# Optimization experiments

Hardware: AMD Instinct MI355X
Metric: run time of the kernel (lower is better)

## Reference

```python
import jax, jax.numpy as jnp
from jax import lax
import numpy as np

B, C, H, W = 32, 3, 224, 224
NUM_CLASSES = 100
K = 3  # kernel size
OUT1 = 32


def _bn(x, g, b, m, v, eps=1e-5):
    # eval-mode batchnorm over channel dim of NCHW
    inv = g / jnp.sqrt(v + eps)
    return x * inv[None, :, None, None] + (b - m * inv)[None, :, None, None]


def _conv(x, w, pad=1):
    return lax.conv_general_dilated(
        x, w, (1, 1), ((pad, pad), (pad, pad)),
        dimension_numbers=('NCHW', 'OIHW', 'NCHW'))


def _maxpool2(x):
    return lax.reduce_window(x, -jnp.inf, lax.max, (1, 1, 2, 2), (1, 1, 2, 2), 'VALID')


def setup_inputs() -> dict:
    key = jax.random.key(0)
    ks = jax.random.split(key, 32)
    n = lambda k, s, sc=0.05: jax.random.normal(k, s, jnp.float32) * sc
    u = lambda k, s: jax.random.uniform(k, s, jnp.float32, 0.5, 1.5)
    inp = {
        'x': jax.random.normal(ks[0], (B, C, H, W), jnp.float32),
        # weight_gen MLP: Linear(3,128)->ReLU->Linear(128,256)->ReLU->Linear(256, 32*3*3*3)
        'w1': n(ks[1], (128, C)), 'b1': n(ks[2], (128,)),
        'w2': n(ks[3], (256, 128)), 'b2': n(ks[4], (256,)),
        'w3': n(ks[5], (OUT1 * C * K * K, 256)), 'b3': n(ks[6], (OUT1 * C * K * K,)),
        # bias_gen: Linear(3, 32)
        'wb': n(ks[7], (OUT1, C)), 'bb': n(ks[8], (OUT1,)),
        'conv2_w': n(ks[9], (64, 32, 3, 3)), 'conv2_b': n(ks[10], (64,)),
        'conv3_w': n(ks[11], (128, 64, 3, 3)), 'conv3_b': n(ks[12], (128,)),
        'bn1_g': 1.0 + n(ks[13], (32,)), 'bn1_b': n(ks[14], (32,)), 'bn1_m': n(ks[15], (32,)), 'bn1_v': u(ks[16], (32,)),
        'bn2_g': 1.0 + n(ks[17], (64,)), 'bn2_b': n(ks[18], (64,)), 'bn2_m': n(ks[19], (64,)), 'bn2_v': u(ks[20], (64,)),
        'bn3_g': 1.0 + n(ks[21], (128,)), 'bn3_b': n(ks[22], (128,)), 'bn3_m': n(ks[23], (128,)), 'bn3_v': u(ks[24], (128,)),
        'fc_w': n(ks[25], (NUM_CLASSES, 128)), 'fc_b': n(ks[26], (NUM_CLASSES,)),
    }
    return inp


def reference(x, w1, b1, w2, b2, w3, b3, wb, bb, conv2_w, conv2_b, conv3_w, conv3_b,
              bn1_g, bn1_b, bn1_m, bn1_v, bn2_g, bn2_b, bn2_m, bn2_v,
              bn3_g, bn3_b, bn3_m, bn3_v, fc_w, fc_b):
    Bx = x.shape[0]
    # DynamicConv2D: channel indicator is all-ones since C == max_in_channels
    ind = jnp.ones((Bx, C), x.dtype)
    h = jax.nn.relu(ind @ w1.T + b1)
    h = jax.nn.relu(h @ w2.T + b2)
    dyn_w = (h @ w3.T + b3).reshape(Bx, OUT1, C, K, K)  # per-sample [O,I,k,k]
    dyn_b = ind @ wb.T + bb                             # per-sample [O]
    # vmap over batch: one single-image conv per sample with its own weights
    y = jax.vmap(lambda xi, wi, bi: _conv(xi[None], wi)[0] + bi[:, None, None])(x, dyn_w, dyn_b)
    y = jax.nn.relu(_bn(y, bn1_g, bn1_b, bn1_m, bn1_v))
    y = _maxpool2(y)
    y = jax.nn.relu(_bn(_conv(y, conv2_w) + conv2_b[None, :, None, None], bn2_g, bn2_b, bn2_m, bn2_v))
    y = _maxpool2(y)
    y = jax.nn.relu(_bn(_conv(y, conv3_w) + conv3_b[None, :, None, None], bn3_g, bn3_b, bn3_m, bn3_v))
    y = y.mean(axis=(2, 3))  # AdaptiveAvgPool2d((1,1)) + flatten
    # dropout is identity in eval
    return y @ fc_w.T + fc_b
```

## Files before the change

kernel.cpp:

```cpp
#include <hip/hip_runtime.h>
#include <hip/hip_bf16.h>

#define BATCH 32
#define HW1 224

typedef __attribute__((ext_vector_type(8))) short short8;
typedef __attribute__((ext_vector_type(4))) float floatx4;

static __device__ __forceinline__ unsigned short f2bf(float f) {
    unsigned int u = __float_as_uint(f);
    unsigned int r = (u + 0x7fffu + ((u >> 16) & 1u)) >> 16;
    return (unsigned short)r;
}

__global__ __launch_bounds__(256) void gen_dynw_repack(
    const float* __restrict__ w1, const float* __restrict__ b1,
    const float* __restrict__ w2, const float* __restrict__ b2,
    const float* __restrict__ w3, const float* __restrict__ b3,
    const float* __restrict__ conv2_w, const float* __restrict__ conv3_w,
    const float* __restrict__ wb, const float* __restrict__ bb,
    const float* __restrict__ conv2_b, const float* __restrict__ conv3_b,
    const float* __restrict__ bn1_g, const float* __restrict__ bn1_b,
    const float* __restrict__ bn1_m, const float* __restrict__ bn1_v,
    const float* __restrict__ bn2_g, const float* __restrict__ bn2_b,
    const float* __restrict__ bn2_m, const float* __restrict__ bn2_v,
    const float* __restrict__ bn3_g, const float* __restrict__ bn3_b,
    const float* __restrict__ bn3_m, const float* __restrict__ bn3_v,
    float* __restrict__ dwt,
    unsigned short* __restrict__ wrep2, unsigned short* __restrict__ wrep3,
    float* __restrict__ bn1_s, float* __restrict__ bn1_t,
    float* __restrict__ bn2_s, float* __restrict__ bn2_t,
    float* __restrict__ bn3_s, float* __restrict__ bn3_t,
    float* __restrict__ feat)
{
    __shared__ float h1s[128];
    __shared__ float h2s[256];
    const int blk = blockIdx.x;
    const int t = threadIdx.x;
    if (blk < 216) {
        if (t < 128) {
            float s = b1[t] + w1[t*3+0] + w1[t*3+1] + w1[t*3+2];
            h1s[t] = fmaxf(s, 0.f);
        }
        __syncthreads();
        {
            float s = b2[t];
            const float* wr = w2 + (size_t)t*128;
#pragma unroll 4
            for (int k = 0; k < 128; k += 4) {
                float4 wv = *(const float4*)(wr + k);
                s = fmaf(wv.x, h1s[k  ], s);
                s = fmaf(wv.y, h1s[k+1], s);
                s = fmaf(wv.z, h1s[k+2], s);
                s = fmaf(wv.w, h1s[k+3], s);
            }
            h2s[t] = fmaxf(s, 0.f);
        }
        __syncthreads();
        const int wave = t >> 6, lane = t & 63;
        const int row = blk*4 + wave;
        float4 wv = *(const float4*)(w3 + (size_t)row*256 + lane*4);
        float4 hv = *(const float4*)&h2s[lane*4];
        float s = wv.x*hv.x + wv.y*hv.y + wv.z*hv.z + wv.w*hv.w;
#pragma unroll
        for (int m = 1; m < 64; m <<= 1) s += __shfl_xor(s, m);
        if (lane == 0) {
            int oc = row / 27, tap = row - oc*27;
            dwt[tap*32 + oc] = s + b3[row];
        }
    } else if (blk < 576) {
        const int i = (blk - 216)*256 + t;
        const int N2 = 9*64*32;
        if (i < N2) {
            int tp = i / (64*32); int rem = i - tp*(64*32);
            int oc = rem >> 5, ic = rem & 31;
            wrep2[i] = f2bf(conv2_w[(oc*32 + ic)*9 + tp]);
        } else {
            int j = i - N2;
            int tp = j / (128*64); int rem = j - tp*(128*64);
            int oc = rem >> 6, ic = rem & 63;
            wrep3[j] = f2bf(conv3_w[(oc*64 + ic)*9 + tp]);
        }
    } else {
        if (t < 32) {
            float dynb = bb[t] + wb[t*3+0] + wb[t*3+1] + wb[t*3+2];
            float s = bn1_g[t] / sqrtf(bn1_v[t] + 1e-5f);
            bn1_s[t] = s;
            bn1_t[t] = (dynb - bn1_m[t]) * s + bn1_b[t];
        }
        if (t < 64) {
            float s = bn2_g[t] / sqrtf(bn2_v[t] + 1e-5f);
            bn2_s[t] = s;
            bn2_t[t] = (conv2_b[t] - bn2_m[t]) * s + bn2_b[t];
        }
        if (t < 128) {
            float s = bn3_g[t] / sqrtf(bn3_v[t] + 1e-5f);
            bn3_s[t] = s;
            bn3_t[t] = (conv3_b[t] - bn3_m[t]) * s + bn3_b[t];
        }
        for (int i = t; i < BATCH*128; i += 256) feat[i] = 0.f;
    }
}

__global__ __launch_bounds__(256) void conv1_pool(
    const float* __restrict__ x, const float* __restrict__ dwt,
    const float* __restrict__ bn_s, const float* __restrict__ bn_t,
    unsigned short* __restrict__ act1)
{
    __shared__ __align__(16) unsigned short sp[18*18*4];
    __shared__ __align__(16) unsigned short swA[32*32];
    __shared__ __align__(16) unsigned short swB[32*32];

    const int tid = threadIdx.x;
    const int bx = blockIdx.x, by = blockIdx.y, b = blockIdx.z;
    const int gx0 = bx*16 - 1, gy0 = by*16 - 1;
    const float* xb = x + (size_t)b * 3 * HW1 * HW1;

    for (int i = tid; i < 1024; i += 256) { swA[i] = 0; swB[i] = 0; }

    for (int i = tid; i < 324; i += 256) {
        int r = i / 18, c = i - r*18;
        int gy = gy0 + r, gx = gx0 + c;
        unsigned short v0 = 0, v1 = 0, v2 = 0;
        if ((unsigned)gy < HW1 && (unsigned)gx < HW1) {
            const float* pp = xb + gy*HW1 + gx;
            v0 = f2bf(pp[0]);
            v1 = f2bf(pp[HW1*HW1]);
            v2 = f2bf(pp[2*HW1*HW1]);
        }
        unsigned int lo = (unsigned int)v0 | ((unsigned int)v1 << 16);
        unsigned int hi = (unsigned int)v2;
        *(uint2*)&sp[i*4] = make_uint2(lo, hi);
    }
    __syncthreads();

    for (int i = tid; i < 864; i += 256) {
        int tap = i >> 5, oc = i & 31;
        int ic = tap / 9, kk = tap - ic*9;
        int ky = kk / 3, kx = kk - ky*3;
        unsigned short v = f2bf(dwt[i]);
        if (kk == 8)      swB[oc*32 + ic] = v;
        else if (kx < 2)  swA[oc*32 + ky*8 + kx*4 + ic] = v;
        else              swA[oc*32 + 3*8  + ky*4 + ic] = v;
    }
    __syncthreads();

    const int lane = tid & 63, wave = tid >> 6;
    const int n = lane & 15, quad = lane >> 4;

    short8 afrA[2], afrB[2];
#pragma unroll
    for (int h = 0; h < 2; ++h) {
        afrA[h] = *(const short8*)&swA[((h*16 + n)*32) + quad*8];
        afrB[h] = *(const short8*)&swB[((h*16 + n)*32) + quad*8];
    }
    float4 sv[2], tv[2];
#pragma unroll
    for (int h = 0; h < 2; ++h) {
        sv[h] = *(const float4*)(bn_s + h*16 + quad*4);
        tv[h] = *(const float4*)(bn_t + h*16 + quad*4);
    }

    union U { short8 s8; uint2 u2[2]; };

    const int y0w = wave*4;
    float ev[2][4];

#pragma unroll
    for (int yi = 0; yi < 4; ++yi) {
        const int y = y0w + yi;
        int r0 = (quad < 3) ? (y + quad) : y;
        int c0 = (quad < 3) ? n : (n + 2);
        int r1 = (quad < 3) ? (y + quad) : (y + 1);
        int c1 = (quad < 3) ? (n + 1) : (n + 2);
        U bf1;
        bf1.u2[0] = *(const uint2*)&sp[(r0*18 + c0)*4];
        bf1.u2[1] = *(const uint2*)&sp[(r1*18 + c1)*4];
        U bf2;
        bf2.u2[0] = *(const uint2*)&sp[((y+2)*18 + (n+2))*4];
        bf2.u2[1] = bf2.u2[0];

        float vr[2][4];
#pragma unroll
        for (int h = 0; h < 2; ++h) {
            floatx4 acc = {0.f, 0.f, 0.f, 0.f};
            acc = __builtin_amdgcn_mfma_f32_16x16x32_bf16(afrA[h], bf1.s8, acc, 0, 0, 0);
            acc = __builtin_amdgcn_mfma_f32_16x16x32_bf16(afrB[h], bf2.s8, acc, 0, 0, 0);
            float sj[4] = {sv[h].x, sv[h].y, sv[h].z, sv[h].w};
            float tj[4] = {tv[h].x, tv[h].y, tv[h].z, tv[h].w};
#pragma unroll
            for (int j = 0; j < 4; ++j)
                vr[h][j] = fmaxf(fmaf(acc[j], sj[j], tj[j]), 0.f);
        }

        if ((yi & 1) == 0) {
#pragma unroll
            for (int h = 0; h < 2; ++h)
#pragma unroll
                for (int j = 0; j < 4; ++j) ev[h][j] = vr[h][j];
        } else {
            int py = by*8 + ((y0w + yi) >> 1);
            int px = bx*8 + (n >> 1);
            unsigned short* dstp =
                act1 + ((size_t)((b*112 + py)*112 + px))*32 + quad*4;
#pragma unroll
            for (int h = 0; h < 2; ++h) {
                unsigned int pk[2];
#pragma unroll
                for (int j = 0; j < 4; ++j) {
                    float m = fmaxf(vr[h][j], ev[h][j]);
                    m = fmaxf(m, __shfl_xor(m, 1));
                    unsigned short us = f2bf(m);
                    if (j & 1) pk[j >> 1] |= ((unsigned int)us) << 16;
                    else       pk[j >> 1]  = us;
                }
                if (!(n & 1)) *(uint2*)(dstp + h*16) = *(uint2*)pk;
            }
        }
    }
}

__global__ __launch_bounds__(256) void conv2_mfma(
    const unsigned short* __restrict__ act1,
    const unsigned short* __restrict__ wrep,
    const float* __restrict__ bn_s, const float* __restrict__ bn_t,
    unsigned short* __restrict__ act2)
{
    constexpr int IC = 32, OC = 64, H = 112;
    __shared__ __align__(16) short lds[4*18*18*8];

    const int tid = threadIdx.x;
    const int b = blockIdx.z;
    const int cx0 = blockIdx.x*16, cy0 = blockIdx.y*16;
    const unsigned short* ab = act1 + (size_t)b*H*H*IC;

    for (int s = tid; s < 4*324; s += 256) {
        int ck = s / 324; int rem = s - ck*324;
        int y = rem / 18, xx = rem - y*18;
        int gy = cy0 - 1 + y, gx = cx0 - 1 + xx;
        uint4 v = {0,0,0,0};
        if ((unsigned)gy < H && (unsigned)gx < H)
            v = *(const uint4*)(ab + (size_t)(gy*H + gx)*IC + ck*8);
        *(uint4*)&lds[s*8] = v;
    }

    const int lane = tid & 63, wave = tid >> 6;
    const int n = lane & 15, quad = lane >> 4;
    const int oc0w = wave * 16;

    short8 afr[9];
#pragma unroll
    for (int t = 0; t < 9; ++t)
        afr[t] = *(const short8*)(wrep + (size_t)(t*OC + oc0w + n)*IC + quad*8);

    float4 sv = *(const float4*)(bn_s + oc0w + quad*4);
    float4 tv = *(const float4*)(bn_t + oc0w + quad*4);
    float sj[4] = {sv.x, sv.y, sv.z, sv.w};
    float tj[4] = {tv.x, tv.y, tv.z, tv.w};

    __syncthreads();

    floatx4 acc[3];
    float ev[4];

#pragma unroll
    for (int r = 0; r < 18; ++r) {
        const short* rp = &lds[((quad*18 + r)*18 + n)*8];
        short8 w0 = *(const short8*)(rp);
        short8 w1 = *(const short8*)(rp + 8);
        short8 w2 = *(const short8*)(rp + 16);

        if (r < 16) {
            floatx4 a = {0.f,0.f,0.f,0.f};
            a = __builtin_amdgcn_mfma_f32_16x16x32_bf16(afr[0], w0, a, 0, 0, 0);
            a = __builtin_amdgcn_mfma_f32_16x16x32_bf16(afr[1], w1, a, 0, 0, 0);
            a = __builtin_amdgcn_mfma_f32_16x16x32_bf16(afr[2], w2, a, 0, 0, 0);
            acc[r % 3] = a;
        }
        if (r >= 1 && r <= 16) {
            int y = r - 1;
            floatx4 a = acc[y % 3];
            a = __builtin_amdgcn_mfma_f32_16x16x32_bf16(afr[3], w0, a, 0, 0, 0);
            a = __builtin_amdgcn_mfma_f32_16x16x32_bf16(afr[4], w1, a, 0, 0, 0);
            a = __builtin_amdgcn_mfma_f32_16x16x32_bf16(afr[5], w2, a, 0, 0, 0);
            acc[y % 3] = a;
        }
        if (r >= 2) {
            int y = r - 2;
            floatx4 a = acc[y % 3];
            a = __builtin_amdgcn_mfma_f32_16x16x32_bf16(afr[6], w0, a, 0, 0, 0);
            a = __builtin_amdgcn_mfma_f32_16x16x32_bf16(afr[7], w1, a, 0, 0, 0);
            a = __builtin_amdgcn_mfma_f32_16x16x32_bf16(afr[8], w2, a, 0, 0, 0);

            float v[4];
#pragma unroll
            for (int j = 0; j < 4; ++j)
                v[j] = fmaxf(fmaf(a[j], sj[j], tj[j]), 0.f);

            if ((y & 1) == 0) {
#pragma unroll
                for (int j = 0; j < 4; ++j) ev[j] = v[j];
            } else {
                unsigned int pk[2];
#pragma unroll
                for (int j = 0; j < 4; ++j) {
                    float m = fmaxf(v[j], ev[j]);
                    m = fmaxf(m, __shfl_xor(m, 1));
                    unsigned short us = f2bf(m);
                    if (j & 1) pk[j >> 1] |= ((unsigned int)us) << 16;
                    else       pk[j >> 1]  = us;
                }
                if (!(n & 1)) {
                    int py = (cy0 >> 1) + (y >> 1), px = (cx0 >> 1) + (n >> 1);
                    unsigned short* dstp =
                        act2 + ((size_t)((b*56 + py)*56 + px))*OC + oc0w + quad*4;
                    *(uint2*)dstp = *(uint2*)pk;
                }
            }
        }
    }
}

__global__ __launch_bounds__(256) void conv3_mfma(
    const unsigned short* __restrict__ act2,
    const unsigned short* __restrict__ wrep,
    const float* __restrict__ bn_s, const float* __restrict__ bn_t,
    float* __restrict__ feat)
{
    constexpr int IC = 64, OC = 128, H = 56;
    __shared__ __align__(16) short lds[8*16*18*8];

    const int tid = threadIdx.x;
    const int b = blockIdx.z >> 1, half = blockIdx.z & 1;
    const int cx0 = blockIdx.x*16, cy0 = blockIdx.y*14;
    const unsigned short* ab = act2 + (size_t)b*H*H*IC;

    for (int s = tid; s < 8*16*18; s += 256) {
        int ck = s / (16*18); int rem = s - ck*(16*18);
        int y = rem / 18, xx = rem - y*18;
        int gy = cy0 - 1 + y, gx = cx0 - 1 + xx;
        uint4 v = {0,0,0,0};
        if ((unsigned)gy < H && (unsigned)gx < H)
            v = *(const uint4*)(ab + (size_t)(gy*H + gx)*IC + ck*8);
        *(uint4*)&lds[s*8] = v;
    }

    const int lane = tid & 63, wave = tid >> 6;
    const int n = lane & 15, quad = lane >> 4;
    const int oc0w = half*64 + wave*16;

    short8 afr[18];
#pragma unroll
    for (int t = 0; t < 9; ++t)
#pragma unroll
        for (int kc = 0; kc < 2; ++kc)
            afr[t*2 + kc] = *(const short8*)(wrep + (size_t)(t*OC + oc0w + n)*IC + kc*32 + quad*8);

    float4 sv = *(const float4*)(bn_s + oc0w + quad*4);
    float4 tv = *(const float4*)(bn_t + oc0w + quad*4);
    float sj[4] = {sv.x, sv.y, sv.z, sv.w};
    float tj[4] = {tv.x, tv.y, tv.z, tv.w};

    __syncthreads();

    float sum[4] = {0.f, 0.f, 0.f, 0.f};
    const bool vx = (cx0 + n) < H;
    floatx4 acc[3];

#pragma unroll
    for (int r = 0; r < 16; ++r) {
        const short* p0 = &lds[((quad*16     + r)*18 + n)*8];
        const short* p1 = &lds[(((4+quad)*16 + r)*18 + n)*8];
        short8 a0 = *(const short8*)(p0);
        short8 a1 = *(const short8*)(p0 + 8);
        short8 a2 = *(const short8*)(p0 + 16);
        short8 b0 = *(const short8*)(p1);
        short8 b1 = *(const short8*)(p1 + 8);
        short8 b2 = *(const short8*)(p1 + 16);

        if (r < 14) {
            floatx4 a = {0.f,0.f,0.f,0.f};
            a = __builtin_amdgcn_mfma_f32_16x16x32_bf16(afr[0], a0, a, 0, 0, 0);
            a = __builtin_amdgcn_mfma_f32_16x16x32_bf16(afr[1], b0, a, 0, 0, 0);
            a = __builtin_amdgcn_mfma_f32_16x16x32_bf16(afr[2], a1, a, 0, 0, 0);
            a = __builtin_amdgcn_mfma_f32_16x16x32_bf16(afr[3], b1, a, 0, 0, 0);
            a = __builtin_amdgcn_mfma_f32_16x16x32_bf16(afr[4], a2, a, 0, 0, 0);
            a = __builtin_amdgcn_mfma_f32_16x16x32_bf16(afr[5], b2, a, 0, 0, 0);
            acc[r % 3] = a;
        }
        if (r >= 1 && r <= 14) {
            int y = r - 1;
            floatx4 a = acc[y % 3];
            a = __builtin_amdgcn_mfma_f32_16x16x32_bf16(afr[6],  a0, a, 0, 0, 0);
            a = __builtin_amdgcn_mfma_f32_16x16x32_bf16(afr[7],  b0, a, 0, 0, 0);
            a = __builtin_amdgcn_mfma_f32_16x16x32_bf16(afr[8],  a1, a, 0, 0, 0);
            a = __builtin_amdgcn_mfma_f32_16x16x32_bf16(afr[9],  b1, a, 0, 0, 0);
            a = __builtin_amdgcn_mfma_f32_16x16x32_bf16(afr[10], a2, a, 0, 0, 0);
            a = __builtin_amdgcn_mfma_f32_16x16x32_bf16(afr[11], b2, a, 0, 0, 0);
            acc[y % 3] = a;
        }
        if (r >= 2) {
            int y = r - 2;
            floatx4 a = acc[y % 3];
            a = __builtin_amdgcn_mfma_f32_16x16x32_bf16(afr[12], a0, a, 0, 0, 0);
            a = __builtin_amdgcn_mfma_f32_16x16x32_bf16(afr[13], b0, a, 0, 0, 0);
            a = __builtin_amdgcn_mfma_f32_16x16x32_bf16(afr[14], a1, a, 0, 0, 0);
            a = __builtin_amdgcn_mfma_f32_16x16x32_bf16(afr[15], b1, a, 0, 0, 0);
            a = __builtin_amdgcn_mfma_f32_16x16x32_bf16(afr[16], a2, a, 0, 0, 0);
            a = __builtin_amdgcn_mfma_f32_16x16x32_bf16(afr[17], b2, a, 0, 0, 0);
            if (vx) {
#pragma unroll
                for (int j = 0; j < 4; ++j)
                    sum[j] += fmaxf(fmaf(a[j], sj[j], tj[j]), 0.f);
            }
        }
    }
#pragma unroll
    for (int j = 0; j < 4; ++j) {
        sum[j] += __shfl_xor(sum[j], 1);
        sum[j] += __shfl_xor(sum[j], 2);
        sum[j] += __shfl_xor(sum[j], 4);
        sum[j] += __shfl_xor(sum[j], 8);
    }
    if (n == 0) {
#pragma unroll
        for (int j = 0; j < 4; ++j)
            atomicAdd(&feat[b*128 + oc0w + quad*4 + j], sum[j]);
    }
}

__global__ __launch_bounds__(256) void fc_kernel(
    const float* __restrict__ feat, const float* __restrict__ fc_w,
    const float* __restrict__ fc_b, float* __restrict__ out)
{
    int i = blockIdx.x * 256 + threadIdx.x;
    if (i >= BATCH*100) return;
    int b = i / 100, n = i - b*100;
    const float* f = feat + b*128;
    const float* w = fc_w + n*128;
    float s = 0.f;
#pragma unroll 4
    for (int k = 0; k < 128; ++k) s = fmaf(f[k], w[k], s);
    out[i] = s * (1.f/3136.f) + fc_b[n];
}

extern "C" void kernel_launch(void* const* d_in, const int* in_sizes, int n_in,
                              void* d_out, int out_size, void* d_ws, size_t ws_size,
                              hipStream_t stream)
{
    const float* x       = (const float*)d_in[0];
    const float* w1      = (const float*)d_in[1];
    const float* b1      = (const float*)d_in[2];
    const float* w2      = (const float*)d_in[3];
    const float* b2      = (const float*)d_in[4];
    const float* w3      = (const float*)d_in[5];
    const float* b3      = (const float*)d_in[6];
    const float* wb      = (const float*)d_in[7];
    const float* bb      = (const float*)d_in[8];
    const float* conv2_w = (const float*)d_in[9];
    const float* conv2_b = (const float*)d_in[10];
    const float* conv3_w = (const float*)d_in[11];
    const float* conv3_b = (const float*)d_in[12];
    const float* bn1_g = (const float*)d_in[13];
    const float* bn1_b = (const float*)d_in[14];
    const float* bn1_m = (const float*)d_in[15];
    const float* bn1_v = (const float*)d_in[16];
    const float* bn2_g = (const float*)d_in[17];
    const float* bn2_b = (const float*)d_in[18];
    const float* bn2_m = (const float*)d_in[19];
    const float* bn2_v = (const float*)d_in[20];
    const float* bn3_g = (const float*)d_in[21];
    const float* bn3_b = (const float*)d_in[22];
    const float* bn3_m = (const float*)d_in[23];
    const float* bn3_v = (const float*)d_in[24];
    const float* fc_w  = (const float*)d_in[25];
    const float* fc_b  = (const float*)d_in[26];
    float* out = (float*)d_out;

    char* wsb = (char*)d_ws;
    float* ws    = (float*)d_ws;
    float* dwt   = ws;
    float* bn1_s = ws + 864;
    float* bn1_t = ws + 896;
    float* bn2_s = ws + 928;
    float* bn2_t = ws + 992;
    float* bn3_s = ws + 1056;
    float* bn3_t = ws + 1184;
    float* feat  = ws + 1312;
    unsigned short* wrep2 = (unsigned short*)(wsb + 32768);
    unsigned short* wrep3 = (unsigned short*)(wsb + 69632);
    unsigned short* act1  = (unsigned short*)(wsb + 262144);
    unsigned short* act2  = (unsigned short*)(wsb + 262144 + 25690112);

    gen_dynw_repack<<<577, 256, 0, stream>>>(
        w1, b1, w2, b2, w3, b3, conv2_w, conv3_w,
        wb, bb, conv2_b, conv3_b,
        bn1_g, bn1_b, bn1_m, bn1_v, bn2_g, bn2_b, bn2_m, bn2_v,
        bn3_g, bn3_b, bn3_m, bn3_v,
        dwt, wrep2, wrep3,
        bn1_s, bn1_t, bn2_s, bn2_t, bn3_s, bn3_t, feat);

    conv1_pool<<<dim3(14, 14, BATCH), 256, 0, stream>>>(
        x, dwt, bn1_s, bn1_t, act1);

    conv2_mfma<<<dim3(7, 7, BATCH), 256, 0, stream>>>(
        act1, wrep2, bn2_s, bn2_t, act2);

    conv3_mfma<<<dim3(4, 4, BATCH*2), 256, 0, stream>>>(
        act2, wrep3, bn3_s, bn3_t, feat);

    fc_kernel<<<(BATCH*100 + 255)/256, 256, 0, stream>>>(feat, fc_w, fc_b, out);
}
```

Baseline: 191.9 us.

## Use direct global-to-LDS loads in conv tiles and parallelize FC and prologue loops

```diff
diff --git a/kernel.cpp b/kernel.cpp
--- a/kernel.cpp
+++ b/kernel.cpp
@@ -11,6 +11,12 @@
     unsigned int u = __float_as_uint(f);
     unsigned int r = (u + 0x7fffu + ((u >> 16) & 1u)) >> 16;
     return (unsigned short)r;
+}
+
+typedef __attribute__((address_space(1))) const unsigned int guint;
+typedef __attribute__((address_space(3))) unsigned int suint;
+static __device__ __forceinline__ void gload_lds16(const void* g, void* l) {
+    __builtin_amdgcn_global_load_lds((guint*)g, (suint*)l, 16, 0, 0);
 }
 
 __global__ __launch_bounds__(256) void gen_dynw_repack(
@@ -44,17 +50,17 @@
         }
         __syncthreads();
         {
-            float s = b2[t];
+            float s0 = b2[t], s1 = 0.f, s2 = 0.f, s3 = 0.f;
             const float* wr = w2 + (size_t)t*128;
 #pragma unroll 4
             for (int k = 0; k < 128; k += 4) {
                 float4 wv = *(const float4*)(wr + k);
-                s = fmaf(wv.x, h1s[k  ], s);
-                s = fmaf(wv.y, h1s[k+1], s);
-                s = fmaf(wv.z, h1s[k+2], s);
-                s = fmaf(wv.w, h1s[k+3], s);
-            }
-            h2s[t] = fmaxf(s, 0.f);
+                s0 = fmaf(wv.x, h1s[k  ], s0);
+                s1 = fmaf(wv.y, h1s[k+1], s1);
+                s2 = fmaf(wv.z, h1s[k+2], s2);
+                s3 = fmaf(wv.w, h1s[k+3], s3);
+            }
+            h2s[t] = fmaxf((s0 + s1) + (s2 + s3), 0.f);
         }
         __syncthreads();
         const int wave = t >> 6, lane = t & 63;
@@ -118,30 +124,46 @@
 
     for (int i = tid; i < 1024; i += 256) { swA[i] = 0; swB[i] = 0; }
 
-    for (int i = tid; i < 324; i += 256) {
-        int r = i / 18, c = i - r*18;
-        int gy = gy0 + r, gx = gx0 + c;
-        unsigned short v0 = 0, v1 = 0, v2 = 0;
-        if ((unsigned)gy < HW1 && (unsigned)gx < HW1) {
-            const float* pp = xb + gy*HW1 + gx;
-            v0 = f2bf(pp[0]);
-            v1 = f2bf(pp[HW1*HW1]);
-            v2 = f2bf(pp[2*HW1*HW1]);
-        }
-        unsigned int lo = (unsigned int)v0 | ((unsigned int)v1 << 16);
-        unsigned int hi = (unsigned int)v2;
-        *(uint2*)&sp[i*4] = make_uint2(lo, hi);
+    float v[2][3];
+#pragma unroll
+    for (int k = 0; k < 2; ++k) {
+        int i = tid + k*256;
+        v[k][0] = 0.f; v[k][1] = 0.f; v[k][2] = 0.f;
+        if (i < 324) {
+            int r = i / 18, c = i - r*18;
+            int gy = gy0 + r, gx = gx0 + c;
+            if ((unsigned)gy < HW1 && (unsigned)gx < HW1) {
+                const float* pp = xb + gy*HW1 + gx;
+                v[k][0] = pp[0];
+                v[k][1] = pp[HW1*HW1];
+                v[k][2] = pp[2*HW1*HW1];
+            }
+        }
+    }
+#pragma unroll
+    for (int k = 0; k < 2; ++k) {
+        int i = tid + k*256;
+        if (i < 324) {
+            unsigned int lo = (unsigned int)f2bf(v[k][0]) |
+                              ((unsigned int)f2bf(v[k][1]) << 16);
+            unsigned int hi = (unsigned int)f2bf(v[k][2]);
+            *(uint2*)&sp[i*4] = make_uint2(lo, hi);
+        }
     }
     __syncthreads();
 
-    for (int i = tid; i < 864; i += 256) {
-        int tap = i >> 5, oc = i & 31;
-        int ic = tap / 9, kk = tap - ic*9;
-        int ky = kk / 3, kx = kk - ky*3;
-        unsigned short v = f2bf(dwt[i]);
-        if (kk == 8)      swB[oc*32 + ic] = v;
-        else if (kx < 2)  swA[oc*32 + ky*8 + kx*4 + ic] = v;
-        else              swA[oc*32 + 3*8  + ky*4 + ic] = v;
+#pragma unroll
+    for (int k = 0; k < 4; ++k) {
+        int i = tid + k*256;
+        if (i < 864) {
+            int tap = i >> 5, oc = i & 31;
+            int ic = tap / 9, kk = tap - ic*9;
+            int ky = kk / 3, kx = kk - ky*3;
+            unsigned short w = f2bf(dwt[i]);
+            if (kk == 8)      swB[oc*32 + ic] = w;
+            else if (kx < 2)  swA[oc*32 + ky*8 + kx*4 + ic] = w;
+            else              swA[oc*32 + 3*8  + ky*4 + ic] = w;
+        }
     }
     __syncthreads();
 
@@ -234,14 +256,27 @@
     const int cx0 = blockIdx.x*16, cy0 = blockIdx.y*16;
     const unsigned short* ab = act1 + (size_t)b*H*H*IC;
 
-    for (int s = tid; s < 4*324; s += 256) {
-        int ck = s / 324; int rem = s - ck*324;
-        int y = rem / 18, xx = rem - y*18;
-        int gy = cy0 - 1 + y, gx = cx0 - 1 + xx;
-        uint4 v = {0,0,0,0};
-        if ((unsigned)gy < H && (unsigned)gx < H)
-            v = *(const uint4*)(ab + (size_t)(gy*H + gx)*IC + ck*8);
-        *(uint4*)&lds[s*8] = v;
+    unsigned bad = 0;
+    {
+        int k = 0;
+        for (int s = tid; s < 4*324; s += 256, ++k) {
+            int ck = s / 324; int rem = s - ck*324;
+            int y = rem / 18, xx = rem - y*18;
+            int gy = cy0 - 1 + y, gx = cx0 - 1 + xx;
+            if (!(((unsigned)gy < H) && ((unsigned)gx < H))) {
+                bad |= 1u << k; gy = 0; gx = 0;
+            }
+            gload_lds16(ab + (size_t)(gy*H + gx)*IC + ck*8, &lds[s*8]);
+        }
+        if (bad) {
+            asm volatile("s_waitcnt vmcnt(0)" ::: "memory");
+            k = 0;
+            for (int s = tid; s < 4*324; s += 256, ++k)
+                if (bad & (1u << k)) {
+                    uint4 z = {0u,0u,0u,0u};
+                    *(uint4*)&lds[s*8] = z;
+                }
+        }
     }
 
     const int lane = tid & 63, wave = tid >> 6;
@@ -335,14 +370,27 @@
     const int cx0 = blockIdx.x*16, cy0 = blockIdx.y*14;
     const unsigned short* ab = act2 + (size_t)b*H*H*IC;
 
-    for (int s = tid; s < 8*16*18; s += 256) {
-        int ck = s / (16*18); int rem = s - ck*(16*18);
-        int y = rem / 18, xx = rem - y*18;
-        int gy = cy0 - 1 + y, gx = cx0 - 1 + xx;
-        uint4 v = {0,0,0,0};
-        if ((unsigned)gy < H && (unsigned)gx < H)
-            v = *(const uint4*)(ab + (size_t)(gy*H + gx)*IC + ck*8);
-        *(uint4*)&lds[s*8] = v;
+    unsigned bad = 0;
+    {
+        int k = 0;
+        for (int s = tid; s < 8*16*18; s += 256, ++k) {
+            int ck = s / (16*18); int rem = s - ck*(16*18);
+            int y = rem / 18, xx = rem - y*18;
+            int gy = cy0 - 1 + y, gx = cx0 - 1 + xx;
+            if (!(((unsigned)gy < H) && ((unsigned)gx < H))) {
+                bad |= 1u << k; gy = 0; gx = 0;
+            }
+            gload_lds16(ab + (size_t)(gy*H + gx)*IC + ck*8, &lds[s*8]);
+        }
+        if (bad) {
+            asm volatile("s_waitcnt vmcnt(0)" ::: "memory");
+            k = 0;
+            for (int s = tid; s < 8*16*18; s += 256, ++k)
+                if (bad & (1u << k)) {
+                    uint4 z = {0u,0u,0u,0u};
+                    *(uint4*)&lds[s*8] = z;
+                }
+        }
     }
 
     const int lane = tid & 63, wave = tid >> 6;
@@ -433,15 +481,23 @@
     const float* __restrict__ feat, const float* __restrict__ fc_w,
     const float* __restrict__ fc_b, float* __restrict__ out)
 {
-    int i = blockIdx.x * 256 + threadIdx.x;
-    if (i >= BATCH*100) return;
-    int b = i / 100, n = i - b*100;
-    const float* f = feat + b*128;
-    const float* w = fc_w + n*128;
-    float s = 0.f;
-#pragma unroll 4
-    for (int k = 0; k < 128; ++k) s = fmaf(f[k], w[k], s);
-    out[i] = s * (1.f/3136.f) + fc_b[n];
+    int g = blockIdx.x * 16 + (threadIdx.x >> 4);
+    int l = threadIdx.x & 15;
+    if (g >= BATCH*100) return;
+    int b = g / 100, n = g - b*100;
+    const float* f = feat + b*128 + l*8;
+    const float* w = fc_w + (size_t)n*128 + l*8;
+    float4 f0 = *(const float4*)(f);
+    float4 f1 = *(const float4*)(f + 4);
+    float4 w0 = *(const float4*)(w);
+    float4 w1 = *(const float4*)(w + 4);
+    float s = f0.x*w0.x + f0.y*w0.y + f0.z*w0.z + f0.w*w0.w
+            + f1.x*w1.x + f1.y*w1.y + f1.z*w1.z + f1.w*w1.w;
+    s += __shfl_xor(s, 1);
+    s += __shfl_xor(s, 2);
+    s += __shfl_xor(s, 4);
+    s += __shfl_xor(s, 8);
+    if (l == 0) out[g] = s * (1.f/3136.f) + fc_b[n];
 }
 
 extern "C" void kernel_launch(void* const* d_in, const int* in_sizes, int n_in,
@@ -509,5 +565,5 @@
     conv3_mfma<<<dim3(4, 4, BATCH*2), 256, 0, stream>>>(
         act2, wrep3, bn3_s, bn3_t, feat);
 
-    fc_kernel<<<(BATCH*100 + 255)/256, 256, 0, stream>>>(feat, fc_w, fc_b, out);
-}
+    fc_kernel<<<200, 256, 0, stream>>>(feat, fc_w, fc_b, out);
+}
```

Result: faster. 182.2 us (-5.1%).
